# Performance work log

Measured on AMD Instinct MI355X. Metric: run time of the kernel, lower is better.

The kernel has to match this reference:

```python
import jax, jax.numpy as jnp
import numpy as np
import math

D_MODEL = 768
NUM_HEADS = 12
HEAD_DIM = D_MODEL // NUM_HEADS
HIDDEN = 3072
EPS = 1e-05
CLAMP = 1e9


def setup_inputs() -> dict:
    key = jax.random.key(0)
    ks = jax.random.split(key, 8)
    s = 0.02
    return {
        "x": jax.random.normal(ks[0], (1, 4096, D_MODEL), dtype=jnp.float32),
        "gamma1": jnp.ones((D_MODEL,), jnp.float32),
        "beta1": jnp.zeros((D_MODEL,), jnp.float32),
        "Wqkv": jax.random.normal(ks[1], (D_MODEL, 3 * D_MODEL), jnp.float32) * s,
        "bqkv": jnp.zeros((3 * D_MODEL,), jnp.float32),
        "Wo": jax.random.normal(ks[2], (D_MODEL, D_MODEL), jnp.float32) * s,
        "bo": jnp.zeros((D_MODEL,), jnp.float32),
        "gamma2": jnp.ones((D_MODEL,), jnp.float32),
        "beta2": jnp.zeros((D_MODEL,), jnp.float32),
        "W1": jax.random.normal(ks[3], (D_MODEL, HIDDEN), jnp.float32) * s,
        "b1": jnp.zeros((HIDDEN,), jnp.float32),
        "W2": jax.random.normal(ks[4], (HIDDEN, D_MODEL), jnp.float32) * s,
        "b2": jnp.zeros((D_MODEL,), jnp.float32),
    }


def layer_norm(x, gamma, beta):
    mean = jnp.mean(x, axis=-1, keepdims=True)
    var = jnp.mean((x - mean) ** 2, axis=-1, keepdims=True)
    y = (x - mean) / jnp.sqrt(var + EPS)
    return gamma * y + beta


def attention_block(x, Wqkv, bqkv, Wo, bo):
    B, S, D = x.shape
    qkv = x @ Wqkv + bqkv                             # [B,S,3D]
    qkv = qkv.reshape(B, S, NUM_HEADS, 3 * HEAD_DIM).transpose(0, 2, 1, 3)  # [B,H,S,3hd]
    q, k, v = jnp.split(qkv, 3, axis=-1)              # each [B,H,S,hd]
    scaled = jnp.einsum("bhqd,bhkd->bhqk", q, k) / math.sqrt(HEAD_DIM)
    causal = jnp.tril(jnp.ones((S, S), dtype=bool))
    scaled = jnp.where(causal, scaled, -jnp.inf)
    scaled = jnp.clip(scaled, -CLAMP, CLAMP)          # torch clamp turns -inf into -1e9
    attn = jax.nn.softmax(scaled, axis=-1)
    vals = jnp.einsum("bhqk,bhkd->bhqd", attn, v)     # [B,H,S,hd]
    vals = vals.transpose(0, 2, 1, 3).reshape(B, S, D)
    return vals @ Wo + bo


def ffn_block(x, W1, b1, W2, b2):
    h = jax.nn.gelu(x @ W1 + b1, approximate=False)
    return h @ W2 + b2


def reference(x, gamma1, beta1, Wqkv, bqkv, Wo, bo, gamma2, beta2, W1, b1, W2, b2):
    x = x + attention_block(layer_norm(x, gamma1, beta1), Wqkv, bqkv, Wo, bo)
    x = x + ffn_block(layer_norm(x, gamma2, beta2), W1, b1, W2, b2)
    return x
```

## Files before the change

### kernel.cpp

```cpp
#include <hip/hip_runtime.h>
#include <hip/hip_bf16.h>
#include <cmath>

using u16 = unsigned short;
typedef __bf16 bf16x8 __attribute__((ext_vector_type(8)));
typedef __bf16 bf16x2 __attribute__((ext_vector_type(2)));
typedef unsigned short u16x8 __attribute__((ext_vector_type(8)));
typedef float f32x4 __attribute__((ext_vector_type(4)));

#define SEQ 4096
#define DM 768
#define NH 12
#define HD 64
#define HID 3072

__device__ __forceinline__ u16 f2bf(float f) {
    union { float f; unsigned u; } v; v.f = f;
    unsigned r = v.u + 0x7fffu + ((v.u >> 16) & 1u);
    return (u16)(r >> 16);
}

__device__ __forceinline__ unsigned pack_bf16(float a, float b) {
    union { bf16x2 v; unsigned u; } c;
    c.v[0] = (__bf16)a; c.v[1] = (__bf16)b;
    return c.u;
}

__device__ __forceinline__ float gelu_exact(float v) {
    float z = fabsf(v) * 0.70710678118654752f;
    float t = __builtin_amdgcn_rcpf(__builtin_fmaf(0.3275911f, z, 1.0f));
    float p = t * __builtin_fmaf(t, __builtin_fmaf(t, __builtin_fmaf(t,
                __builtin_fmaf(t, 1.061405429f, -1.453152027f),
                1.421413741f), -0.284496736f), 0.254829592f);
    float e = __builtin_amdgcn_exp2f(-z * z * 1.44269504088896341f);
    float erfv = __builtin_fmaf(-p, e, 1.0f);
    erfv = (v < 0.0f) ? -erfv : erfv;
    return 0.5f * v * (1.0f + erfv);
}

__device__ __forceinline__ int swz64(int row, int k) {
    return (row << 6) | ((((k >> 3) ^ row) & 7) << 3) | (k & 7);
}
__device__ __forceinline__ int swz128(int row, int k) {
    return (row << 7) | ((((k >> 3) ^ row) & 15) << 3) | (k & 7);
}

__global__ void transpose_to_bf16(const float* __restrict__ W, u16* __restrict__ Wt,
                                  int K, int N) {
    __shared__ float tile[32][33];
    int kb = blockIdx.y * 32, nb = blockIdx.x * 32;
    int tx = threadIdx.x, ty = threadIdx.y;
#pragma unroll
    for (int i = 0; i < 32; i += 8)
        tile[ty + i][tx] = W[(size_t)(kb + ty + i) * N + nb + tx];
    __syncthreads();
#pragma unroll
    for (int i = 0; i < 32; i += 8)
        Wt[(size_t)(nb + ty + i) * K + kb + tx] = f2bf(tile[tx][ty + i]);
}

__global__ __launch_bounds__(256) void ln_kernel(const float* __restrict__ x,
                                                 const float* __restrict__ g,
                                                 const float* __restrict__ b,
                                                 u16* __restrict__ y) {
    int row = blockIdx.x, t = threadIdx.x;
    const float* xr = x + (size_t)row * DM;
    float v0 = xr[t], v1 = xr[t + 256], v2 = xr[t + 512];
    float s = v0 + v1 + v2;
#pragma unroll
    for (int m = 32; m; m >>= 1) s += __shfl_xor(s, m);
    __shared__ float red[4], red2[4];
    int wid = t >> 6, lane = t & 63;
    if (lane == 0) red[wid] = s;
    __syncthreads();
    float mean = (red[0] + red[1] + red[2] + red[3]) * (1.0f / DM);
    float d0 = v0 - mean, d1 = v1 - mean, d2 = v2 - mean;
    float q = d0 * d0 + d1 * d1 + d2 * d2;
#pragma unroll
    for (int m = 32; m; m >>= 1) q += __shfl_xor(q, m);
    if (lane == 0) red2[wid] = q;
    __syncthreads();
    float var = (red2[0] + red2[1] + red2[2] + red2[3]) * (1.0f / DM);
    float rstd = rsqrtf(var + 1e-5f);
    y[(size_t)row * DM + t]       = f2bf(d0 * rstd * g[t]       + b[t]);
    y[(size_t)row * DM + t + 256] = f2bf(d1 * rstd * g[t + 256] + b[t + 256]);
    y[(size_t)row * DM + t + 512] = f2bf(d2 * rstd * g[t + 512] + b[t + 512]);
}

template<int TM>
__global__ __launch_bounds__(256) void gemm_bf16(
    const u16* __restrict__ A, const u16* __restrict__ Bt,
    const float* __restrict__ bias, const float* __restrict__ resid,
    float* __restrict__ outF, u16* __restrict__ outB,
    int M, int N, int K, int gelu) {
    constexpr int AP = TM / 32;
    constexpr int NF = (TM == 128) ? 4 : 2;
    __shared__ __align__(16) u16 As[2][TM * 64];
    __shared__ __align__(16) u16 Bs[2][128 * 64];
    int tid = threadIdx.x;
    int lane = tid & 63, wid = tid >> 6;
    int lr = lane & 15, hi = lane >> 4;
    int wrow = (TM == 128) ? (wid >> 1) * 64 : 0;
    int wcol = (TM == 128) ? (wid & 1) * 64 : wid * 32;
    int m0 = blockIdx.y * TM, n0 = blockIdx.x * 128;

    f32x4 acc[4][NF] = {};
    int srow = tid >> 3;
    int sk = (tid & 7) << 3;
    const u16* Ag = A + (size_t)(m0 + srow) * K + sk;
    const u16* Bg = Bt + (size_t)(n0 + srow) * K + sk;

    u16x8 ar[AP], br[4];
    auto LOAD = [&](int kt) {
#pragma unroll
        for (int p = 0; p < AP; ++p)
            ar[p] = *reinterpret_cast<const u16x8*>(Ag + (size_t)p * 32 * K + kt);
#pragma unroll
        for (int p = 0; p < 4; ++p)
            br[p] = *reinterpret_cast<const u16x8*>(Bg + (size_t)p * 32 * K + kt);
    };
    auto WRITE = [&](int buf) {
#pragma unroll
        for (int p = 0; p < AP; ++p)
            *reinterpret_cast<u16x8*>(&As[buf][swz64(srow + p * 32, sk)]) = ar[p];
#pragma unroll
        for (int p = 0; p < 4; ++p)
            *reinterpret_cast<u16x8*>(&Bs[buf][swz64(srow + p * 32, sk)]) = br[p];
    };

    int NT = K >> 6;
    LOAD(0);
    WRITE(0);
#pragma unroll 2
    for (int t = 0; t < NT; ++t) {
        if (t + 1 < NT) LOAD((t + 1) << 6);
        __syncthreads();
        const u16* as = &As[t & 1][0];
        const u16* bs = &Bs[t & 1][0];
#pragma unroll
        for (int ks = 0; ks < 2; ++ks) {
            bf16x8 af[4], bfr[NF];
#pragma unroll
            for (int m = 0; m < 4; ++m)
                af[m] = *reinterpret_cast<const bf16x8*>(&as[swz64(wrow + m * 16 + lr, ks * 32 + hi * 8)]);
#pragma unroll
            for (int n = 0; n < NF; ++n)
                bfr[n] = *reinterpret_cast<const bf16x8*>(&bs[swz64(wcol + n * 16 + lr, ks * 32 + hi * 8)]);
            __builtin_amdgcn_s_setprio(1);
#pragma unroll
            for (int m = 0; m < 4; ++m)
#pragma unroll
                for (int n = 0; n < NF; ++n)
                    acc[m][n] = __builtin_amdgcn_mfma_f32_16x16x32_bf16(af[m], bfr[n], acc[m][n], 0, 0, 0);
            __builtin_amdgcn_s_setprio(0);
        }
        if (t + 1 < NT) WRITE((t + 1) & 1);
    }
#pragma unroll
    for (int m = 0; m < 4; ++m) {
#pragma unroll
        for (int n = 0; n < NF; ++n) {
            int col = n0 + wcol + n * 16 + lr;
            float bv = bias[col];
#pragma unroll
            for (int r = 0; r < 4; ++r) {
                int row = m0 + wrow + m * 16 + hi * 4 + r;
                float v = acc[m][n][r] + bv;
                if (gelu) v = gelu_exact(v);
                if (resid) v += resid[(size_t)row * N + col];
                if (outF) outF[(size_t)row * N + col] = v;
                if (outB) outB[(size_t)row * N + col] = f2bf(v);
            }
        }
    }
}

__global__ __launch_bounds__(256, 3) void attn_kernel(const u16* __restrict__ qkv,
                                                      u16* __restrict__ attn) {
    __shared__ __align__(16) u16 Ks[128 * 64];
    __shared__ __align__(16) u16 Vt[64 * 128];
    int tid = threadIdx.x;
    int lane = tid & 63, w = tid >> 6;
    int lr = lane & 15, hi = lane >> 4;
    int upper = hi >> 1;
    const float SCL = 0.125f * 1.44269504088896340736f;

    int bid = blockIdx.x;
    int h = bid % NH;
    int qb = (SEQ / 64 - 1) - bid / NH;

    int qrow = qb * 64 + w * 16 + lr;
    bf16x8 qf[2];
#pragma unroll
    for (int ks = 0; ks < 2; ++ks)
        qf[ks] = *reinterpret_cast<const bf16x8*>(&qkv[(size_t)qrow * 2304 + h * 192 + ks * 32 + hi * 8]);

    f32x4 acc[4] = {};
    float m_run = -INFINITY, l_run = 0.0f;

    int nt = (qb * 64 + 64 + 127) >> 7;
    for (int kb = 0; kb < nt; ++kb) {
        __syncthreads();
#pragma unroll
        for (int p = 0; p < 4; ++p) {
            int kvr = (tid >> 3) + p * 32;
            int c = (tid & 7) << 3;
            u16x8 kv = *reinterpret_cast<const u16x8*>(
                &qkv[(size_t)(kb * 128 + kvr) * 2304 + h * 192 + 64 + c]);
            *reinterpret_cast<u16x8*>(&Ks[swz64(kvr, c)]) = kv;
        }
        {
            int d = tid & 63;
            int kvq = (tid >> 6) * 32;
            const u16* vb = &qkv[(size_t)(kb * 128 + kvq) * 2304 + h * 192 + 128 + d];
#pragma unroll
            for (int g = 0; g < 4; ++g) {
                u16x8 vv;
#pragma unroll
                for (int j = 0; j < 8; ++j)
                    vv[j] = vb[(size_t)(g * 8 + j) * 2304];
                *reinterpret_cast<u16x8*>(&Vt[swz128(d, kvq + g * 8)]) = vv;
            }
        }
        __syncthreads();

        f32x4 s[8] = {};
        __builtin_amdgcn_s_setprio(1);
#pragma unroll
        for (int ks = 0; ks < 2; ++ks) {
#pragma unroll
            for (int n = 0; n < 8; ++n) {
                bf16x8 kf = *reinterpret_cast<const bf16x8*>(&Ks[swz64(n * 16 + lr, ks * 32 + hi * 8)]);
                s[n] = __builtin_amdgcn_mfma_f32_16x16x32_bf16(kf, qf[ks], s[n], 0, 0, 0);
            }
        }
        __builtin_amdgcn_s_setprio(0);
        float sv[8][4];
#pragma unroll
        for (int n = 0; n < 8; ++n) {
            sv[n][0] = s[n][0]; sv[n][1] = s[n][1]; sv[n][2] = s[n][2]; sv[n][3] = s[n][3];
        }
        if (kb == nt - 1) {
#pragma unroll
            for (int n = 0; n < 8; ++n)
#pragma unroll
                for (int r = 0; r < 4; ++r) {
                    int kv = kb * 128 + n * 16 + hi * 4 + r;
                    if (kv > qrow) sv[n][r] = -3.0e38f;
                }
        }
        float t8[8];
#pragma unroll
        for (int n = 0; n < 8; ++n)
            t8[n] = fmaxf(fmaxf(sv[n][0], sv[n][1]), fmaxf(sv[n][2], sv[n][3]));
        float mx = fmaxf(fmaxf(fmaxf(t8[0], t8[1]), fmaxf(t8[2], t8[3])),
                         fmaxf(fmaxf(t8[4], t8[5]), fmaxf(t8[6], t8[7])));
        mx = fmaxf(mx, __shfl_xor(mx, 16));
        mx = fmaxf(mx, __shfl_xor(mx, 32));
        float mxs = mx * SCL;
        if (!__all(mxs <= m_run + 8.0f)) {
            float mnew = fmaxf(m_run, mxs);
            float alpha = __builtin_amdgcn_exp2f(m_run - mnew);
            l_run *= alpha;
#pragma unroll
            for (int n2 = 0; n2 < 4; ++n2)
#pragma unroll
                for (int r = 0; r < 4; ++r) acc[n2][r] *= alpha;
            m_run = mnew;
        }
        float rs = 0.0f;
#pragma unroll
        for (int n = 0; n < 8; ++n) {
            float p0 = __builtin_amdgcn_exp2f(__builtin_fmaf(sv[n][0], SCL, -m_run));
            float p1 = __builtin_amdgcn_exp2f(__builtin_fmaf(sv[n][1], SCL, -m_run));
            float p2 = __builtin_amdgcn_exp2f(__builtin_fmaf(sv[n][2], SCL, -m_run));
            float p3 = __builtin_amdgcn_exp2f(__builtin_fmaf(sv[n][3], SCL, -m_run));
            sv[n][0] = p0; sv[n][1] = p1; sv[n][2] = p2; sv[n][3] = p3;
            rs += (p0 + p1) + (p2 + p3);
        }
        rs += __shfl_xor(rs, 16);
        rs += __shfl_xor(rs, 32);
        l_run += rs;

        unsigned pk0[8], pk1[8];
#pragma unroll
        for (int n = 0; n < 8; ++n) {
            pk0[n] = pack_bf16(sv[n][0], sv[n][1]);
            pk1[n] = pack_bf16(sv[n][2], sv[n][3]);
        }
        int src0 = lr + ((hi & 1) << 5);
        int src1 = src0 + 16;
#pragma unroll
        for (int ks = 0; ks < 4; ++ks) {
            union { unsigned w4[4]; bf16x8 v; } pf;
            {
                unsigned a0 = __shfl(pk0[2 * ks], src0), b0 = __shfl(pk0[2 * ks + 1], src0);
                unsigned a1 = __shfl(pk1[2 * ks], src0), b1 = __shfl(pk1[2 * ks + 1], src0);
                unsigned a2 = __shfl(pk0[2 * ks], src1), b2 = __shfl(pk0[2 * ks + 1], src1);
                unsigned a3 = __shfl(pk1[2 * ks], src1), b3 = __shfl(pk1[2 * ks + 1], src1);
                pf.w4[0] = upper ? b0 : a0;
                pf.w4[1] = upper ? b1 : a1;
                pf.w4[2] = upper ? b2 : a2;
                pf.w4[3] = upper ? b3 : a3;
            }
            __builtin_amdgcn_s_setprio(1);
#pragma unroll
            for (int n2 = 0; n2 < 4; ++n2) {
                bf16x8 vf = *reinterpret_cast<const bf16x8*>(&Vt[swz128(n2 * 16 + lr, ks * 32 + hi * 8)]);
                acc[n2] = __builtin_amdgcn_mfma_f32_16x16x32_bf16(vf, pf.v, acc[n2], 0, 0, 0);
            }
            __builtin_amdgcn_s_setprio(0);
        }
    }
    float inv = 1.0f / l_run;
#pragma unroll
    for (int n2 = 0; n2 < 4; ++n2) {
#pragma unroll
        for (int r = 0; r < 4; ++r) {
            int dcol = h * 64 + n2 * 16 + hi * 4 + r;
            attn[(size_t)qrow * DM + dcol] = f2bf(acc[n2][r] * inv);
        }
    }
}

extern "C" void kernel_launch(void* const* d_in, const int* in_sizes, int n_in,
                              void* d_out, int out_size, void* d_ws, size_t ws_size,
                              hipStream_t stream) {
    const float* x      = (const float*)d_in[0];
    const float* gamma1 = (const float*)d_in[1];
    const float* beta1  = (const float*)d_in[2];
    const float* Wqkv   = (const float*)d_in[3];
    const float* bqkv   = (const float*)d_in[4];
    const float* Wo     = (const float*)d_in[5];
    const float* bo     = (const float*)d_in[6];
    const float* gamma2 = (const float*)d_in[7];
    const float* beta2  = (const float*)d_in[8];
    const float* W1     = (const float*)d_in[9];
    const float* b1     = (const float*)d_in[10];
    const float* W2     = (const float*)d_in[11];
    const float* b2     = (const float*)d_in[12];

    char* ws = (char*)d_ws;
    size_t off = 0;
    u16* WqkvT = (u16*)(ws + off); off += (size_t)2304 * 768 * 2;
    u16* WoT   = (u16*)(ws + off); off += (size_t)768 * 768 * 2;
    u16* W1T   = (u16*)(ws + off); off += (size_t)3072 * 768 * 2;
    u16* W2T   = (u16*)(ws + off); off += (size_t)768 * 3072 * 2;
    u16* B1    = (u16*)(ws + off); off += (size_t)SEQ * DM * 2;
    u16* Q     = (u16*)(ws + off); off += (size_t)SEQ * HID * 2;
    float* x1  = (float*)(ws + off); off += (size_t)SEQ * DM * 4;

    dim3 tb(32, 8);
    transpose_to_bf16<<<dim3(2304 / 32, 768 / 32), tb, 0, stream>>>(Wqkv, WqkvT, 768, 2304);
    transpose_to_bf16<<<dim3(768 / 32, 768 / 32), tb, 0, stream>>>(Wo, WoT, 768, 768);
    transpose_to_bf16<<<dim3(3072 / 32, 768 / 32), tb, 0, stream>>>(W1, W1T, 768, 3072);
    transpose_to_bf16<<<dim3(768 / 32, 3072 / 32), tb, 0, stream>>>(W2, W2T, 3072, 768);

    ln_kernel<<<SEQ, 256, 0, stream>>>(x, gamma1, beta1, B1);
    gemm_bf16<128><<<dim3(2304 / 128, SEQ / 128), 256, 0, stream>>>(B1, WqkvT, bqkv, nullptr, nullptr, Q, SEQ, 2304, 768, 0);
    attn_kernel<<<dim3((SEQ / 64) * NH), 256, 0, stream>>>(Q, B1);
    gemm_bf16<64><<<dim3(768 / 128, SEQ / 64), 256, 0, stream>>>(B1, WoT, bo, x, x1, nullptr, SEQ, 768, 768, 0);
    ln_kernel<<<SEQ, 256, 0, stream>>>(x1, gamma2, beta2, B1);
    gemm_bf16<128><<<dim3(3072 / 128, SEQ / 128), 256, 0, stream>>>(B1, W1T, b1, nullptr, nullptr, Q, SEQ, 3072, 768, 1);
    gemm_bf16<64><<<dim3(768 / 128, SEQ / 64), 256, 0, stream>>>(Q, W2T, b2, x1, (float*)d_out, nullptr, SEQ, 768, 3072, 0);
}
```

Measured before the change: 248.9 us.

## Split causal attention KV range into chunks with separate combine kernel

Splits each attention query block's KV loop into chunks of up to 16 KV tiles, writing unnormalized partial outputs plus running max/sum to workspace (aliased on x1), then a combine kernel merges the chunks with log-sum-exp rescaling and normalizes. The aim is to even out the causal triangle's per-block work so long-row blocks no longer dominate the tail. In exchange it adds an extra launch, workspace round-trip traffic, and bf16 rounding of the partial outputs before combining.

After: 278.3 us. 1.12x slower.

```diff
diff --git a/kernel.cpp b/kernel.cpp
--- a/kernel.cpp
+++ b/kernel.cpp
@@ -13,11 +13,16 @@
 #define NH 12
 #define HD 64
 #define HID 3072
+#define CHT 16
 
 __device__ __forceinline__ u16 f2bf(float f) {
     union { float f; unsigned u; } v; v.f = f;
     unsigned r = v.u + 0x7fffu + ((v.u >> 16) & 1u);
     return (u16)(r >> 16);
+}
+
+__device__ __forceinline__ float bf2f(u16 a) {
+    union { unsigned u; float f; } v; v.u = ((unsigned)a) << 16; return v.f;
 }
 
 __device__ __forceinline__ unsigned pack_bf16(float a, float b) {
@@ -175,8 +180,13 @@
     }
 }
 
-__global__ __launch_bounds__(256, 3) void attn_kernel(const u16* __restrict__ qkv,
-                                                      u16* __restrict__ attn) {
+__device__ __forceinline__ int chunk_cum(int qb) {
+    return (qb < 32) ? qb : 32 + ((qb - 32) << 1);
+}
+
+__global__ __launch_bounds__(256, 3) void attn_chunk(const u16* __restrict__ qkv,
+                                                     u16* __restrict__ Opart,
+                                                     float* __restrict__ ml) {
     __shared__ __align__(16) u16 Ks[128 * 64];
     __shared__ __align__(16) u16 Vt[64 * 128];
     int tid = threadIdx.x;
@@ -185,9 +195,13 @@
     int upper = hi >> 1;
     const float SCL = 0.125f * 1.44269504088896340736f;
 
-    int bid = blockIdx.x;
-    int h = bid % NH;
-    int qb = (SEQ / 64 - 1) - bid / NH;
+    int c = blockIdx.x;
+    int qb = 63 - blockIdx.y;
+    int h = blockIdx.z;
+    int nt = (qb >> 1) + 1;
+    int kb0 = c * CHT;
+    if (kb0 >= nt) return;
+    int kbend = min(nt, kb0 + CHT);
 
     int qrow = qb * 64 + w * 16 + lr;
     bf16x8 qf[2];
@@ -198,16 +212,15 @@
     f32x4 acc[4] = {};
     float m_run = -INFINITY, l_run = 0.0f;
 
-    int nt = (qb * 64 + 64 + 127) >> 7;
-    for (int kb = 0; kb < nt; ++kb) {
+    for (int kb = kb0; kb < kbend; ++kb) {
         __syncthreads();
 #pragma unroll
         for (int p = 0; p < 4; ++p) {
             int kvr = (tid >> 3) + p * 32;
-            int c = (tid & 7) << 3;
+            int cc = (tid & 7) << 3;
             u16x8 kv = *reinterpret_cast<const u16x8*>(
-                &qkv[(size_t)(kb * 128 + kvr) * 2304 + h * 192 + 64 + c]);
-            *reinterpret_cast<u16x8*>(&Ks[swz64(kvr, c)]) = kv;
+                &qkv[(size_t)(kb * 128 + kvr) * 2304 + h * 192 + 64 + cc]);
+            *reinterpret_cast<u16x8*>(&Ks[swz64(kvr, cc)]) = kv;
         }
         {
             int d = tid & 63;
@@ -312,15 +325,71 @@
             __builtin_amdgcn_s_setprio(0);
         }
     }
-    float inv = 1.0f / l_run;
+    int p = h * 96 + chunk_cum(qb) + c;
+    u16* op = Opart + (size_t)p * 4096;
+    int row = w * 16 + lr;
 #pragma unroll
     for (int n2 = 0; n2 < 4; ++n2) {
-#pragma unroll
-        for (int r = 0; r < 4; ++r) {
-            int dcol = h * 64 + n2 * 16 + hi * 4 + r;
-            attn[(size_t)qrow * DM + dcol] = f2bf(acc[n2][r] * inv);
-        }
-    }
+        unsigned lo = pack_bf16(acc[n2][0], acc[n2][1]);
+        unsigned hi2 = pack_bf16(acc[n2][2], acc[n2][3]);
+        uint2 pr; pr.x = lo; pr.y = hi2;
+        *reinterpret_cast<uint2*>(&op[row * 64 + n2 * 16 + hi * 4]) = pr;
+    }
+    if (hi == 0) {
+        float2 v; v.x = m_run; v.y = l_run;
+        *reinterpret_cast<float2*>(&ml[(size_t)p * 128 + row * 2]) = v;
+    }
+}
+
+__global__ __launch_bounds__(256) void attn_combine(const u16* __restrict__ Opart,
+                                                    const float* __restrict__ ml,
+                                                    u16* __restrict__ attn) {
+    int qb = blockIdx.x, h = blockIdx.y, tid = threadIdx.x;
+    int nc = (qb >> 5) + 1;
+    int pbase = h * 96 + chunk_cum(qb);
+    int row = tid >> 2, dq = (tid & 3) << 4;
+
+    float m0 = ml[(size_t)pbase * 128 + row * 2];
+    float l0 = ml[(size_t)pbase * 128 + row * 2 + 1];
+    const u16* o0 = &Opart[(size_t)pbase * 4096 + row * 64 + dq];
+    float O[16];
+    float linv;
+    if (nc == 2) {
+        float m1 = ml[(size_t)(pbase + 1) * 128 + row * 2];
+        float l1 = ml[(size_t)(pbase + 1) * 128 + row * 2 + 1];
+        const u16* o1 = &Opart[(size_t)(pbase + 1) * 4096 + row * 64 + dq];
+        float ms = fmaxf(m0, m1);
+        float a0 = __builtin_amdgcn_exp2f(m0 - ms);
+        float a1 = __builtin_amdgcn_exp2f(m1 - ms);
+        linv = 1.0f / (a0 * l0 + a1 * l1);
+        u16x8 u0a = *reinterpret_cast<const u16x8*>(o0);
+        u16x8 u0b = *reinterpret_cast<const u16x8*>(o0 + 8);
+        u16x8 u1a = *reinterpret_cast<const u16x8*>(o1);
+        u16x8 u1b = *reinterpret_cast<const u16x8*>(o1 + 8);
+#pragma unroll
+        for (int j = 0; j < 8; ++j) {
+            O[j]     = a0 * bf2f(u0a[j]) + a1 * bf2f(u1a[j]);
+            O[j + 8] = a0 * bf2f(u0b[j]) + a1 * bf2f(u1b[j]);
+        }
+    } else {
+        linv = 1.0f / l0;
+        u16x8 u0a = *reinterpret_cast<const u16x8*>(o0);
+        u16x8 u0b = *reinterpret_cast<const u16x8*>(o0 + 8);
+#pragma unroll
+        for (int j = 0; j < 8; ++j) {
+            O[j] = bf2f(u0a[j]);
+            O[j + 8] = bf2f(u0b[j]);
+        }
+    }
+    u16x8 outa, outb;
+#pragma unroll
+    for (int j = 0; j < 8; ++j) {
+        outa[j] = f2bf(O[j] * linv);
+        outb[j] = f2bf(O[j + 8] * linv);
+    }
+    u16* dst = &attn[(size_t)(qb * 64 + row) * DM + h * 64 + dq];
+    *reinterpret_cast<u16x8*>(dst) = outa;
+    *reinterpret_cast<u16x8*>(dst + 8) = outb;
 }
 
 extern "C" void kernel_launch(void* const* d_in, const int* in_sizes, int n_in,
@@ -350,6 +419,9 @@
     u16* Q     = (u16*)(ws + off); off += (size_t)SEQ * HID * 2;
     float* x1  = (float*)(ws + off); off += (size_t)SEQ * DM * 4;
 
+    u16* Opart = (u16*)x1;
+    float* ml  = (float*)((char*)x1 + (size_t)1152 * 4096 * 2);
+
     dim3 tb(32, 8);
     transpose_to_bf16<<<dim3(2304 / 32, 768 / 32), tb, 0, stream>>>(Wqkv, WqkvT, 768, 2304);
     transpose_to_bf16<<<dim3(768 / 32, 768 / 32), tb, 0, stream>>>(Wo, WoT, 768, 768);
@@ -358,7 +430,8 @@
 
     ln_kernel<<<SEQ, 256, 0, stream>>>(x, gamma1, beta1, B1);
     gemm_bf16<128><<<dim3(2304 / 128, SEQ / 128), 256, 0, stream>>>(B1, WqkvT, bqkv, nullptr, nullptr, Q, SEQ, 2304, 768, 0);
-    attn_kernel<<<dim3((SEQ / 64) * NH), 256, 0, stream>>>(Q, B1);
+    attn_chunk<<<dim3(2, 64, NH), 256, 0, stream>>>(Q, Opart, ml);
+    attn_combine<<<dim3(64, NH), 256, 0, stream>>>(Opart, ml, B1);
     gemm_bf16<64><<<dim3(768 / 128, SEQ / 64), 256, 0, stream>>>(B1, WoT, bo, x, x1, nullptr, SEQ, 768, 768, 0);
     ln_kernel<<<SEQ, 256, 0, stream>>>(x1, gamma2, beta2, B1);
     gemm_bf16<128><<<dim3(3072 / 128, SEQ / 128), 256, 0, stream>>>(B1, W1T, b1, nullptr, nullptr, Q, SEQ, 3072, 768, 1);
```
